# Kernel tuning notes

Hardware: AMD Instinct MI355X
Metric: run time of the kernel (lower is better)

The kernel has to match this reference:

```python
import jax, jax.numpy as jnp
import numpy as np

L = 6        # num_coupling_layers
T_DIM = 64   # t_dim
HALF = T_DIM // 2
COND = 128   # cond_dim
HID = 1024   # hidden_dim
B = 32768


def setup_inputs() -> dict:
    key = jax.random.key(0)
    ks = jax.random.split(key, 8)
    s_in = 1.0 / np.sqrt(HALF + COND)
    s_h = 1.0 / np.sqrt(HID)
    T = jax.random.normal(ks[0], (B, T_DIM), dtype=jnp.float32)
    cond = jax.random.normal(ks[1], (B, COND), dtype=jnp.float32)
    W1 = jax.random.normal(ks[2], (L, HALF + COND, HID), dtype=jnp.float32) * s_in
    b1 = jnp.zeros((L, HID), dtype=jnp.float32)
    W2 = jax.random.normal(ks[3], (L, HID, HID), dtype=jnp.float32) * s_h
    b2 = jnp.zeros((L, HID), dtype=jnp.float32)
    W3 = jax.random.normal(ks[4], (L, HID, 2 * HALF), dtype=jnp.float32) * s_h
    b3 = jnp.zeros((L, 2 * HALF), dtype=jnp.float32)
    return {"T": T, "cond": cond, "W1": W1, "b1": b1, "W2": W2, "b2": b2, "W3": W3, "b3": b3}


def reference(T, cond, W1, b1, W2, b2, W3, b3):
    # Conditional normalizing flow: 6 affine coupling layers with alternating
    # contiguous half masks. Even layers transform the first half, odd the second.
    def mlp(h, i):
        x = jax.nn.relu(h @ W1[i] + b1[i])
        x = jax.nn.relu(x @ W2[i] + b2[i])
        return x @ W3[i] + b3[i]

    z = T
    log_det = jnp.zeros(T.shape[0], dtype=T.dtype)
    for i in range(L):
        if i % 2 == 0:
            masked, unmasked = z[:, :HALF], z[:, HALF:]
        else:
            masked, unmasked = z[:, HALF:], z[:, :HALF]
        params = mlp(jnp.concatenate([unmasked, cond], axis=1), i)
        s = jnp.tanh(params[:, :HALF])
        t_shift = params[:, HALF:]
        y_masked = masked * jnp.exp(s) + t_shift
        if i % 2 == 0:
            z = jnp.concatenate([y_masked, unmasked], axis=1)
        else:
            z = jnp.concatenate([unmasked, y_masked], axis=1)
        log_det = log_det + jnp.sum(s, axis=1)
    return z, log_det
```

## Files before the change

### kernel.cpp

```cpp
#include <hip/hip_runtime.h>
#include <hip/hip_fp16.h>
#include <stdint.h>

typedef _Float16 f16;
typedef _Float16 f16x8 __attribute__((ext_vector_type(8)));
typedef float f32x4 __attribute__((ext_vector_type(4)));

#define NB 32768
#define LAYERS 6
#define AK 160
#define HID 1024

__device__ __forceinline__ void async_copy16(const void* g, void* l) {
  __builtin_amdgcn_global_load_lds(
      (const __attribute__((address_space(1))) void*)g,
      (__attribute__((address_space(3))) void*)l, 16, 0, 0);
}

__device__ __forceinline__ void wtrans_tile(const float* __restrict__ W,
                                            f16* __restrict__ Wt,
                                            const int K_, const int N_,
                                            const int bx, const int by,
                                            const int bz, float (*t)[65])
{
  const long off = (long)bz * K_ * N_;
  const float* Wl = W + off;
  f16* Wtl = Wt + off;
  const int k0 = by * 64, n0 = bx * 64;
  const int tx = threadIdx.x & 63, ty4 = threadIdx.x >> 6;
#pragma unroll
  for (int r = ty4; r < 64; r += 4) {
    const int k = k0 + r;
    if (k < K_) t[r][tx] = Wl[(long)k * N_ + n0 + tx];
  }
  __syncthreads();
  const int k = k0 + tx;
  if (k < K_) {
#pragma unroll
    for (int r = ty4; r < 64; r += 4) {
      const int n = n0 + r;
      Wtl[(long)n * K_ + k] = (f16)t[tx][r];
    }
  }
}

__global__ void prep_all(const float* __restrict__ T, const float* __restrict__ cond,
                         const float* __restrict__ W1, const float* __restrict__ W2,
                         const float* __restrict__ W3,
                         float* __restrict__ z, float* __restrict__ ld,
                         f16* __restrict__ A,
                         f16* __restrict__ W1t, f16* __restrict__ W2t,
                         f16* __restrict__ W3t)
{
  __shared__ float t[64][65];
  const int b = blockIdx.x;
  if (b < 2048) {
    const int S1 = NB * 64;
    const int S2 = S1 + NB;
    const int S3 = S2 + NB * 32;
    const int S4 = S3 + NB * 128;
    for (int i = b * blockDim.x + threadIdx.x; i < S4; i += 2048 * blockDim.x) {
      if (i < S1) {
        z[i] = T[i];
      } else if (i < S2) {
        ld[i - S1] = 0.0f;
      } else if (i < S3) {
        int r = i - S2;
        int row = r >> 5, j = r & 31;
        A[(size_t)row * AK + j] = (f16)T[row * 64 + 32 + j];
      } else {
        int r = i - S3;
        int row = r >> 7, j = r & 127;
        A[(size_t)row * AK + 32 + j] = (f16)cond[r];
      }
    }
  } else if (b < 2048 + 288) {
    const int l = b - 2048;
    wtrans_tile(W1, W1t, AK, 1024, l % 16, (l / 16) % 3, l / 48, t);
  } else if (b < 2048 + 288 + 1536) {
    const int l = b - (2048 + 288);
    wtrans_tile(W2, W2t, HID, 1024, l % 16, (l / 16) % 16, l / 256, t);
  } else {
    const int l = b - (2048 + 288 + 1536);
    wtrans_tile(W3, W3t, HID, 64, 0, l % 16, l / 16, t);
  }
}

__global__ __launch_bounds__(256, 2)
void gemm1_full(const f16* __restrict__ A,
                const f16* __restrict__ Wt,
                const float* __restrict__ bias,
                f16* __restrict__ C)
{
  __shared__ __align__(16) f16 As[128 * 160];
  __shared__ __align__(16) f16 Bs[128 * 160];
  const int tid  = threadIdx.x;
  const int lane = tid & 63;
  const int wave = tid >> 6;
  const int c15  = lane & 15;
  const int quad = lane >> 4;
  const int wm = (wave & 1) * 64;
  const int wn = (wave >> 1) * 64;

  const int b = blockIdx.x;
  const int x = b & 7, i = b >> 3;
  const long rowStart = (long)(x * 32 + (i >> 3)) * 128;
  const long colStart = (long)(i & 7) * 128;

  const f16* Ab = A  + rowStart * AK;
  const f16* Bb = Wt + colStart * AK;

#pragma unroll
  for (int it = 0; it < 10; ++it) {
    const int f = it * 256 + tid;
    const int row = f / 20;
    const int ch  = f - row * 20;
    const int chs = ch ^ ((row >> 1) & 3);
    async_copy16(Ab + (long)row * AK + chs * 8, &As[0] + (long)f * 8);
    async_copy16(Bb + (long)row * AK + chs * 8, &Bs[0] + (long)f * 8);
  }
  __syncthreads();

  f32x4 acc[4][4] = {};
#pragma unroll
  for (int kt = 0; kt < 5; ++kt) {
    f16x8 a[4], bf[4];
#pragma unroll
    for (int mi = 0; mi < 4; ++mi) {
      const int R = wm + mi * 16 + c15;
      a[mi] = *(const f16x8*)&As[(R * 20 + kt * 4 + (quad ^ ((R >> 1) & 3))) * 8];
    }
#pragma unroll
    for (int ni = 0; ni < 4; ++ni) {
      const int R = wn + ni * 16 + c15;
      bf[ni] = *(const f16x8*)&Bs[(R * 20 + kt * 4 + (quad ^ ((R >> 1) & 3))) * 8];
    }
#pragma unroll
    for (int mi = 0; mi < 4; ++mi)
#pragma unroll
      for (int ni = 0; ni < 4; ++ni)
        acc[mi][ni] = __builtin_amdgcn_mfma_f32_16x16x32_f16(
            a[mi], bf[ni], acc[mi][ni], 0, 0, 0);
  }

  __syncthreads();
  f16* Lp = &As[0] + wave * 4096;
  const int erow = lane >> 3;
  const int ec   = lane & 7;
#pragma unroll
  for (int ni = 0; ni < 4; ++ni) {
    const long gn = colStart + wn + ni * 16 + c15;
    const float bv = bias[gn];
    const int lc = ni * 16 + c15;
#pragma unroll
    for (int mi = 0; mi < 4; ++mi) {
#pragma unroll
      for (int r = 0; r < 4; ++r) {
        const int R = mi * 16 + quad * 4 + r;
        float v = acc[mi][ni][r] + bv;
        Lp[R * 64 + (((lc >> 3) ^ (quad << 1)) << 3) + (lc & 7)] = (f16)fmaxf(v, 0.0f);
      }
    }
  }
#pragma unroll
  for (int it = 0; it < 8; ++it) {
    const int R = it * 8 + erow;
    const int phys = ec ^ (((R >> 2) & 3) << 1);
    f16x8 rowv = *(const f16x8*)&Lp[R * 64 + (phys << 3)];
    *(f16x8*)&C[(rowStart + wm + R) * HID + colStart + wn + ec * 8] = rowv;
  }
}

__global__ __launch_bounds__(512, 2)
void gemm2_ep(const f16* __restrict__ A,
              const f16* __restrict__ Wt,
              const float* __restrict__ bias,
              f16* __restrict__ C)
{
  __shared__ __align__(16) f16 As[2][16384];
  __shared__ __align__(16) f16 Bs[2][16384];

  const int tid  = threadIdx.x;
  const int lane = tid & 63;
  const int wave = tid >> 6;
  const int c15  = lane & 15;
  const int quad = lane >> 4;
  const int wm = (wave >> 2) * 128;
  const int wn = (wave & 3) * 64;

  const int b = blockIdx.x;
  const int wgid = (b & 7) * 64 + (b >> 3);
  const long rowStart = (long)(wgid >> 2) * 256;
  const long colStart = (long)(wgid & 3) * 256;

  const f16* Ab = A  + rowStart * HID;
  const f16* Bb = Wt + colStart * HID;

  const int rh0 = tid >> 3;
  const int ch0 = tid & 7;
  const long g0 = (long)rh0 * HID + ((ch0 ^ (rh0 & 7)) << 3);
  const long g1 = (long)(64 + rh0) * HID + ((ch0 ^ ((64 + rh0) & 7)) << 3);
  const int l0 = tid << 3;
  const int l1 = (512 + tid) << 3;

  auto stageA = [&](int kt2, int h, int sel) {
    const f16* src = Ab + (long)h * 128 * HID + (long)kt2 * 64;
    f16* dst = &As[sel][h * 8192];
    async_copy16(src + g0, dst + l0);
    async_copy16(src + g1, dst + l1);
  };
  auto stageB = [&](int kt2, int h, int sel) {
    const f16* src = Bb + (long)h * 128 * HID + (long)kt2 * 64;
    f16* dst = &Bs[sel][h * 8192];
    async_copy16(src + g0, dst + l0);
    async_copy16(src + g1, dst + l1);
  };

  stageA(0, 0, 0); stageA(0, 1, 0);
  stageB(0, 0, 0); stageB(0, 1, 0);
  stageB(1, 0, 1); stageA(1, 0, 1);
  asm volatile("s_waitcnt vmcnt(4)" ::: "memory");
  __builtin_amdgcn_s_barrier();
  __builtin_amdgcn_sched_barrier(0);

  f32x4 acc[8][4] = {};

#pragma unroll 2
  for (int kt = 0; kt < 16; ++kt) {
    const int sel = kt & 1;
    const f16* as = &As[sel][0];
    const f16* bs = &Bs[sel][0];
    const bool s1 = (kt + 1 < 16);
    const bool s2 = (kt + 2 < 16);
    f16x8 a0[4][2], a1[4][2], b0[2][2], b1[2][2];

#pragma unroll
    for (int mi = 0; mi < 4; ++mi) {
      const int r = wm + mi * 16 + c15;
#pragma unroll
      for (int ks = 0; ks < 2; ++ks)
        a0[mi][ks] = *(const f16x8*)&as[r * 64 + ((((ks << 2) + quad) ^ (r & 7)) << 3)];
    }
#pragma unroll
    for (int ni = 0; ni < 2; ++ni) {
      const int r = wn + ni * 16 + c15;
#pragma unroll
      for (int ks = 0; ks < 2; ++ks)
        b0[ni][ks] = *(const f16x8*)&bs[r * 64 + ((((ks << 2) + quad) ^ (r & 7)) << 3)];
    }
    if (s1) stageA(kt + 1, 1, sel ^ 1);
    __builtin_amdgcn_s_barrier();
    asm volatile("s_waitcnt lgkmcnt(0)" ::: "memory");
    __builtin_amdgcn_sched_barrier(0);
    __builtin_amdgcn_s_setprio(1);
#pragma unroll
    for (int mi = 0; mi < 4; ++mi)
#pragma unroll
      for (int ni = 0; ni < 2; ++ni)
#pragma unroll
        for (int ks = 0; ks < 2; ++ks)
          acc[mi][ni] = __builtin_amdgcn_mfma_f32_16x16x32_f16(
              a0[mi][ks], b0[ni][ks], acc[mi][ni], 0, 0, 0);
    __builtin_amdgcn_s_setprio(0);
    __builtin_amdgcn_sched_barrier(0);
    __builtin_amdgcn_s_barrier();

#pragma unroll
    for (int ni = 0; ni < 2; ++ni) {
      const int r = wn + 32 + ni * 16 + c15;
#pragma unroll
      for (int ks = 0; ks < 2; ++ks)
        b1[ni][ks] = *(const f16x8*)&bs[r * 64 + ((((ks << 2) + quad) ^ (r & 7)) << 3)];
    }
    if (s1) stageB(kt + 1, 1, sel ^ 1);
    __builtin_amdgcn_s_barrier();
    asm volatile("s_waitcnt lgkmcnt(0)" ::: "memory");
    __builtin_amdgcn_sched_barrier(0);
    __builtin_amdgcn_s_setprio(1);
#pragma unroll
    for (int mi = 0; mi < 4; ++mi)
#pragma unroll
      for (int ni = 0; ni < 2; ++ni)
#pragma unroll
        for (int ks = 0; ks < 2; ++ks)
          acc[mi][2 + ni] = __builtin_amdgcn_mfma_f32_16x16x32_f16(
              a0[mi][ks], b1[ni][ks], acc[mi][2 + ni], 0, 0, 0);
    __builtin_amdgcn_s_setprio(0);
    __builtin_amdgcn_sched_barrier(0);
    __builtin_amdgcn_s_barrier();

#pragma unroll
    for (int mi = 0; mi < 4; ++mi) {
      const int r = wm + 64 + mi * 16 + c15;
#pragma unroll
      for (int ks = 0; ks < 2; ++ks)
        a1[mi][ks] = *(const f16x8*)&as[r * 64 + ((((ks << 2) + quad) ^ (r & 7)) << 3)];
    }
    if (s2) stageB(kt + 2, 0, sel);
    __builtin_amdgcn_s_barrier();
    asm volatile("s_waitcnt lgkmcnt(0)" ::: "memory");
    __builtin_amdgcn_sched_barrier(0);
    __builtin_amdgcn_s_setprio(1);
#pragma unroll
    for (int mi = 0; mi < 4; ++mi)
#pragma unroll
      for (int ni = 0; ni < 2; ++ni)
#pragma unroll
        for (int ks = 0; ks < 2; ++ks)
          acc[4 + mi][ni] = __builtin_amdgcn_mfma_f32_16x16x32_f16(
              a1[mi][ks], b0[ni][ks], acc[4 + mi][ni], 0, 0, 0);
    __builtin_amdgcn_s_setprio(0);
    __builtin_amdgcn_sched_barrier(0);
    __builtin_amdgcn_s_barrier();

    if (s2) stageA(kt + 2, 0, sel);
    __builtin_amdgcn_s_setprio(1);
#pragma unroll
    for (int mi = 0; mi < 4; ++mi)
#pragma unroll
      for (int ni = 0; ni < 2; ++ni)
#pragma unroll
        for (int ks = 0; ks < 2; ++ks)
          acc[4 + mi][2 + ni] = __builtin_amdgcn_mfma_f32_16x16x32_f16(
              a1[mi][ks], b1[ni][ks], acc[4 + mi][2 + ni], 0, 0, 0);
    __builtin_amdgcn_s_setprio(0);
    if (s2) {
      asm volatile("s_waitcnt vmcnt(4)" ::: "memory");
    } else if (s1) {
      asm volatile("s_waitcnt vmcnt(0)" ::: "memory");
    }
    __builtin_amdgcn_sched_barrier(0);
    __builtin_amdgcn_s_barrier();
  }

  f16* Lp = &As[0][0] + wave * 1024;
  const int erow = lane >> 3;
  const int ec   = lane & 7;
  const int ecol8 = ec * 8;
  const long gcol = colStart + wn;
  const int q0x = ((erow >> 2) & 3) << 1;
  const int q1x = (((8 + erow) >> 2) & 3) << 1;
#pragma unroll
  for (int mii = 0; mii < 8; ++mii) {
    const int mof = (mii >> 2) * 64 + (mii & 3) * 16;
#pragma unroll
    for (int nii = 0; nii < 4; ++nii) {
      const int nof = (nii >> 1) * 32 + (nii & 1) * 16;
      const float bv = bias[gcol + nof + c15];
      const int lc = nof + c15;
#pragma unroll
      for (int r = 0; r < 4; ++r) {
        float v = acc[mii][nii][r] + bv;
        Lp[(quad * 4 + r) * 64 + (((lc >> 3) ^ (quad << 1)) << 3) + (lc & 7)]
            = (f16)fmaxf(v, 0.0f);
      }
    }
    f16x8 row0 = *(const f16x8*)&Lp[erow * 64 + ((ec ^ q0x) << 3)];
    f16x8 row1 = *(const f16x8*)&Lp[(8 + erow) * 64 + ((ec ^ q1x) << 3)];
    const long gm0 = rowStart + wm + mof + erow;
    *(f16x8*)&C[gm0 * HID + gcol + ecol8] = row0;
    *(f16x8*)&C[(gm0 + 8) * HID + gcol + ecol8] = row1;
  }
}

__global__ __launch_bounds__(256, 2)
void gemm3_coupling(const f16* __restrict__ X2, const f16* __restrict__ W3t,
                    const float* __restrict__ b3, float* __restrict__ z,
                    float* __restrict__ log_det, f16* __restrict__ Anext,
                    const int maskoff)
{
  __shared__ __align__(16) f16 As[2][64 * 64];
  __shared__ __align__(16) f16 Bs[2][64 * 64];
  const int tid = threadIdx.x;
  const int wave = tid >> 6, lane = tid & 63;
  const int c15 = lane & 15, quad = lane >> 4;
  const int wm = wave * 16;
  const long rowStart = (long)blockIdx.x * 64;

  const f16* Ab = X2 + rowStart * HID;
  const int brow = tid >> 3;
  const int bkc  = ((tid & 7) ^ (brow & 7)) * 8;

  f32x4 acc[4] = {};

  auto stage = [&](int c, int sel) {
    const long kb = (long)c * 64;
#pragma unroll
    for (int q = 0; q < 2; ++q) {
      async_copy16(Ab  + (long)(q * 32 + brow) * HID + kb + bkc,
                   &As[sel][0] + (q * 256 + wave * 64) * 8);
      async_copy16(W3t + (long)(q * 32 + brow) * HID + kb + bkc,
                   &Bs[sel][0] + (q * 256 + wave * 64) * 8);
    }
  };

  stage(0, 0);
  for (int c = 0; c < 16; ++c) {
    __syncthreads();
    if (c + 1 < 16) stage(c + 1, (c + 1) & 1);
    const f16* as = &As[c & 1][0];
    const f16* bs = &Bs[c & 1][0];

#pragma unroll
    for (int s = 0; s < 2; ++s) {
      const int Ra = wm + c15;
      f16x8 a = *(const f16x8*)&as[(Ra * 8 + ((s * 4 + quad) ^ (Ra & 7))) * 8];
      f16x8 bf[4];
#pragma unroll
      for (int ni = 0; ni < 4; ++ni) {
        const int R = ni * 16 + c15;
        bf[ni] = *(const f16x8*)&bs[(R * 8 + ((s * 4 + quad) ^ (R & 7))) * 8];
      }
#pragma unroll
      for (int ni = 0; ni < 4; ++ni)
        acc[ni] = __builtin_amdgcn_mfma_f32_16x16x32_f16(a, bf[ni], acc[ni], 0, 0, 0);
    }
  }

  float sp[4] = {0.0f, 0.0f, 0.0f, 0.0f};
#pragma unroll
  for (int ni = 0; ni < 2; ++ni) {
    const int j = ni * 16 + c15;
    const float bs = b3[j];
    const float bt = b3[32 + j];
#pragma unroll
    for (int r = 0; r < 4; ++r) {
      const long gm = rowStart + wm + quad * 4 + r;
      const float sv = acc[ni][r] + bs;
      const float e2 = __expf(2.0f * sv);
      const float s  = 1.0f - 2.0f / (e2 + 1.0f);
      const float tv = acc[ni + 2][r] + bt;
      const float m  = z[gm * 64 + maskoff + j];
      const float y  = fmaf(m, __expf(s), tv);
      z[gm * 64 + maskoff + j] = y;
      Anext[gm * AK + j] = (f16)y;
      sp[r] += s;
    }
  }
#pragma unroll
  for (int r = 0; r < 4; ++r) {
    float v = sp[r];
    v += __shfl_xor(v, 1);
    v += __shfl_xor(v, 2);
    v += __shfl_xor(v, 4);
    v += __shfl_xor(v, 8);
    if (c15 == 0) {
      const long gm = rowStart + wm + quad * 4 + r;
      log_det[gm] += v;
    }
  }
}

extern "C" void kernel_launch(void* const* d_in, const int* in_sizes, int n_in,
                              void* d_out, int out_size, void* d_ws, size_t ws_size,
                              hipStream_t stream) {
  (void)in_sizes; (void)n_in; (void)out_size; (void)ws_size;
  const float* T    = (const float*)d_in[0];
  const float* cond = (const float*)d_in[1];
  const float* W1   = (const float*)d_in[2];
  const float* b1   = (const float*)d_in[3];
  const float* W2   = (const float*)d_in[4];
  const float* b2   = (const float*)d_in[5];
  const float* W3   = (const float*)d_in[6];
  const float* b3   = (const float*)d_in[7];

  float* z  = (float*)d_out;
  float* ld = z + (size_t)NB * 64;

  f16* A   = (f16*)d_ws;
  f16* X1  = A   + (size_t)NB * AK;
  f16* X2  = X1  + (size_t)NB * HID;
  f16* W1t = X2  + (size_t)NB * HID;
  f16* W2t = W1t + (size_t)6 * 1024 * 160;
  f16* W3t = W2t + ((size_t)6 << 20);

  prep_all<<<3968, 256, 0, stream>>>(T, cond, W1, W2, W3,
                                     z, ld, A, W1t, W2t, W3t);

  const int g1 = (NB / 128) * (HID / 128);
  const int g2 = (NB / 256) * (HID / 256);
  for (int l = 0; l < LAYERS; ++l) {
    gemm1_full<<<g1, 256, 0, stream>>>(A, W1t + (size_t)l * 1024 * AK,
                                       b1 + l * 1024, X1);
    gemm2_ep<<<g2, 512, 0, stream>>>(X1, W2t + ((size_t)l << 20),
                                     b2 + l * 1024, X2);
    const int maskoff = (l & 1) ? 32 : 0;
    gemm3_coupling<<<NB / 64, 256, 0, stream>>>(X2, W3t + (size_t)l * 64 * 1024,
                                                b3 + l * 64, z, ld, A, maskoff);
  }
}
```

Measured before the change: 751.0 us.

## Prefetch two stages ahead in final GEMM and drop LDS-staged epilogue

The final-layer GEMM now keeps two async global-to-LDS stages in flight, preloading fragments into registers before issuing the next stage, with explicit waitcnt and barriers in place of __syncthreads. This is meant to hide global load latency behind the MFMA work. Separately, the hidden-layer GEMM epilogue now writes scalar f16 values straight to global memory instead of staging them through LDS for coalesced 16-byte stores. That removes a barrier and the LDS round trip, but the global writes become narrow and poorly coalesced.

```diff
diff --git a/kernel.cpp b/kernel.cpp
--- a/kernel.cpp
+++ b/kernel.cpp
@@ -143,31 +143,20 @@
             a[mi], bf[ni], acc[mi][ni], 0, 0, 0);
   }
 
-  __syncthreads();
-  f16* Lp = &As[0] + wave * 4096;
-  const int erow = lane >> 3;
-  const int ec   = lane & 7;
 #pragma unroll
   for (int ni = 0; ni < 4; ++ni) {
     const long gn = colStart + wn + ni * 16 + c15;
     const float bv = bias[gn];
-    const int lc = ni * 16 + c15;
 #pragma unroll
     for (int mi = 0; mi < 4; ++mi) {
 #pragma unroll
       for (int r = 0; r < 4; ++r) {
-        const int R = mi * 16 + quad * 4 + r;
+        const long gm = rowStart + wm + mi * 16 + quad * 4 + r;
         float v = acc[mi][ni][r] + bv;
-        Lp[R * 64 + (((lc >> 3) ^ (quad << 1)) << 3) + (lc & 7)] = (f16)fmaxf(v, 0.0f);
+        v = fmaxf(v, 0.0f);
+        C[gm * HID + gn] = (f16)v;
       }
     }
-  }
-#pragma unroll
-  for (int it = 0; it < 8; ++it) {
-    const int R = it * 8 + erow;
-    const int phys = ec ^ (((R >> 2) & 3) << 1);
-    f16x8 rowv = *(const f16x8*)&Lp[R * 64 + (phys << 3)];
-    *(f16x8*)&C[(rowStart + wm + R) * HID + colStart + wn + ec * 8] = rowv;
   }
 }
 
@@ -395,26 +384,42 @@
   };
 
   stage(0, 0);
+  stage(1, 1);
+  asm volatile("s_waitcnt vmcnt(4)" ::: "memory");
+  __builtin_amdgcn_s_barrier();
+
   for (int c = 0; c < 16; ++c) {
-    __syncthreads();
-    if (c + 1 < 16) stage(c + 1, (c + 1) & 1);
-    const f16* as = &As[c & 1][0];
-    const f16* bs = &Bs[c & 1][0];
-
+    const int sel = c & 1;
+    const f16* as = &As[sel][0];
+    const f16* bs = &Bs[sel][0];
+
+    f16x8 av[2], bv[2][4];
 #pragma unroll
     for (int s = 0; s < 2; ++s) {
       const int Ra = wm + c15;
-      f16x8 a = *(const f16x8*)&as[(Ra * 8 + ((s * 4 + quad) ^ (Ra & 7))) * 8];
-      f16x8 bf[4];
+      av[s] = *(const f16x8*)&as[(Ra * 8 + ((s * 4 + quad) ^ (Ra & 7))) * 8];
 #pragma unroll
       for (int ni = 0; ni < 4; ++ni) {
         const int R = ni * 16 + c15;
-        bf[ni] = *(const f16x8*)&bs[(R * 8 + ((s * 4 + quad) ^ (R & 7))) * 8];
+        bv[s][ni] = *(const f16x8*)&bs[(R * 8 + ((s * 4 + quad) ^ (R & 7))) * 8];
       }
+    }
+    asm volatile("s_waitcnt lgkmcnt(0)" ::: "memory");
+    __builtin_amdgcn_s_barrier();
+    if (c + 2 < 16) stage(c + 2, sel);
+
+#pragma unroll
+    for (int s = 0; s < 2; ++s)
 #pragma unroll
       for (int ni = 0; ni < 4; ++ni)
-        acc[ni] = __builtin_amdgcn_mfma_f32_16x16x32_f16(a, bf[ni], acc[ni], 0, 0, 0);
-    }
+        acc[ni] = __builtin_amdgcn_mfma_f32_16x16x32_f16(av[s], bv[s][ni],
+                                                         acc[ni], 0, 0, 0);
+    if (c + 2 < 16) {
+      asm volatile("s_waitcnt vmcnt(4)" ::: "memory");
+    } else if (c + 1 < 16) {
+      asm volatile("s_waitcnt vmcnt(0)" ::: "memory");
+    }
+    __builtin_amdgcn_s_barrier();
   }
 
   float sp[4] = {0.0f, 0.0f, 0.0f, 0.0f};
```

Measured after the change: 728.5 us. -3.0%, faster.
